# Optimization experiments

Measured on AMD Instinct MI355X. Metric: run time of the kernel, lower is better.

## Reference

```python
import jax, jax.numpy as jnp
import numpy as np

T = 8          # number of adapter tasks
H = 1024       # hidden_size
I = 4096       # intermediate_size (bert dense input)
D = H // 16    # adapter bottleneck (reduction_factor=16)
B, S = 8, 512
EPS = 1e-12    # BERT LayerNorm eps


def _layernorm(x, g, b):
    mu = jnp.mean(x, axis=-1, keepdims=True)
    var = jnp.mean(jnp.square(x - mu), axis=-1, keepdims=True)
    return (x - mu) * jax.lax.rsqrt(var + EPS) * g + b


def setup_inputs() -> dict:
    key = jax.random.key(0)
    ks = jax.random.split(key, 14)
    std = 0.02
    inp = {
        "hidden_states": jax.random.normal(ks[0], (B, S, I), jnp.float32),
        "input_tensor": jax.random.normal(ks[1], (B, S, H), jnp.float32),
        "dense_w": jax.random.normal(ks[2], (H, I), jnp.float32) * std,
        "dense_b": jnp.zeros((H,), jnp.float32),
        "ln_g": jnp.ones((H,), jnp.float32),
        "ln_b": jnp.zeros((H,), jnp.float32),
        "down_w": jax.random.normal(ks[3], (T, D, H), jnp.float32) * std,
        "down_b": jnp.zeros((T, D), jnp.float32),
        "up_w": jax.random.normal(ks[4], (T, H, D), jnp.float32) * std,
        "up_b": jnp.zeros((T, H), jnp.float32),
        "key_w": jax.random.normal(ks[5], (H, H), jnp.float32) * std,
        "key_b": jnp.zeros((H,), jnp.float32),
        "query_w": jax.random.normal(ks[6], (H, H), jnp.float32) * std,
        "query_b": jnp.zeros((H,), jnp.float32),
        # value init: near-zero with identity diagonal
        "value_w": jnp.full((H, H), 1e-6, jnp.float32).at[jnp.arange(H), jnp.arange(H)].set(1.0),
    }
    return inp


def reference(hidden_states, input_tensor, dense_w, dense_b, ln_g, ln_b,
              down_w, down_b, up_w, up_b, key_w, key_b, query_w, query_b, value_w):
    # dense: [B,S,I] @ [H,I]^T -> [B,S,H]   (dropout = identity in eval)
    h = jnp.einsum('bsi,hi->bsh', hidden_states, dense_w) + dense_b
    prenorm = input_tensor + h
    adapter_in = _layernorm(prenorm, ln_g, ln_b)
    # batched per-task adapters: down-project, relu, up-project -> [T,B,S,H]
    down = jax.nn.relu(jnp.einsum('bsh,tdh->tbsd', adapter_in, down_w)
                       + down_b[:, None, None, :])
    adapter_out = jnp.einsum('tbsd,thd->tbsh', down, up_w) + up_b[:, None, None, :]
    # fusion attention over task axis T
    key = jnp.einsum('tbsh,kh->tbsk', adapter_out, key_w) + key_b
    value = jnp.einsum('tbsh,vh->tbsv', adapter_out + h[None], value_w)
    query = jnp.einsum('bsh,qh->bsq', prenorm, query_w) + query_b
    scores = jnp.sum(query[None] * key, axis=-1, keepdims=True)  # [T,B,S,1]
    probs = jax.nn.softmax(scores, axis=0)
    fusion = jnp.sum(probs * value, axis=0)                       # [B,S,H]
    return _layernorm(input_tensor + fusion, ln_g, ln_b)
```

## Files before the change

### kernel.cpp

```cpp
#include <hip/hip_runtime.h>
#include <cstdint>
#include <cstddef>

typedef float   f32x4 __attribute__((ext_vector_type(4)));
typedef _Float16 f16x8 __attribute__((ext_vector_type(8)));
typedef _Float16 f16x4 __attribute__((ext_vector_type(4)));

#define TOK  4096
#define HID  1024
#define IDIM 4096

#define GLDS16(gp, lp) __builtin_amdgcn_global_load_lds(                      \
    (const __attribute__((address_space(1))) void*)(gp),                      \
    (__attribute__((address_space(3))) void*)(lp), 16, 0, 0)


__global__ __launch_bounds__(256, 4) void gemm_dense(
    const _Float16* __restrict__ A, const _Float16* __restrict__ B,
    int K, int Kchunk, float* __restrict__ part)
{
    __shared__ _Float16 lA[4096];
    __shared__ _Float16 lB[4096];
    const int tid  = threadIdx.x;
    const int lane = tid & 63;
    const int wave = tid >> 6;
    const int m0   = blockIdx.x * 128;
    const int n0   = blockIdx.y * 128;
    const int kz0  = blockIdx.z * Kchunk;
    const int wM   = (wave & 1) * 64;
    const int wN   = (wave >> 1) * 64;

    const int srow = lane >> 2;
    const int scol = ((lane & 3) ^ ((lane >> 3) & 3)) * 8;
    const _Float16* gA0 = A + (size_t)(m0 + wave * 32 + srow) * K + kz0 + scol;
    const _Float16* gA1 = gA0 + (size_t)16 * K;
    const _Float16* gB0 = B + (size_t)(n0 + wave * 32 + srow) * K + kz0 + scol;
    const _Float16* gB1 = gB0 + (size_t)16 * K;
    _Float16* sA0 = lA + wave * 1024;
    _Float16* sB0 = lB + wave * 1024;

    f32x4 acc[4][4] = {};
    const int fr  = lane & 15;
    const int khr = lane >> 4;
    const int kxo = (khr ^ ((fr >> 1) & 3)) * 8;

    for (int k = 0; k < Kchunk; k += 32) {
        GLDS16(gA0 + k, sA0);
        GLDS16(gA1 + k, sA0 + 512);
        GLDS16(gB0 + k, sB0);
        GLDS16(gB1 + k, sB0 + 512);
        __syncthreads();
        f16x8 afr[4], bfr[4];
#pragma unroll
        for (int mi = 0; mi < 4; ++mi)
            afr[mi] = *(const f16x8*)(lA + (wM + mi * 16 + fr) * 32 + kxo);
#pragma unroll
        for (int ni = 0; ni < 4; ++ni)
            bfr[ni] = *(const f16x8*)(lB + (wN + ni * 16 + fr) * 32 + kxo);
#pragma unroll
        for (int mi = 0; mi < 4; ++mi)
#pragma unroll
            for (int ni = 0; ni < 4; ++ni)
                acc[mi][ni] = __builtin_amdgcn_mfma_f32_16x16x32_f16(
                    afr[mi], bfr[ni], acc[mi][ni], 0, 0, 0);
        __syncthreads();
    }

    float* dst = part + (size_t)blockIdx.z * TOK * HID;
    const int cn = lane & 15;
    const int rq = (lane >> 4) * 4;
#pragma unroll
    for (int mi = 0; mi < 4; ++mi)
#pragma unroll
        for (int r = 0; r < 4; ++r) {
            const int m = m0 + wM + mi * 16 + rq + r;
#pragma unroll
            for (int ni = 0; ni < 4; ++ni) {
                const int n = n0 + wN + ni * 16 + cn;
                dst[(size_t)m * HID + n] = acc[mi][ni][r];
            }
        }
}

template <int MODE>
__global__ __launch_bounds__(1024, 4) void gemm_w32(
    const _Float16* __restrict__ Ah, const _Float16* __restrict__ B,
    int K, int Ncols,
    float* __restrict__ outF, _Float16* __restrict__ outH,
    const float* __restrict__ bias, const float* __restrict__ addv,
    const float* __restrict__ probs, const float* __restrict__ upb,
    const _Float16* __restrict__ A2, const _Float16* __restrict__ B2,
    _Float16* __restrict__ outH2)
{
    __shared__ _Float16 lA[4096];
    __shared__ _Float16 lB[4096];
    const int tid  = threadIdx.x;
    const int lane = tid & 63;
    const int wave = tid >> 6;
    const int m0   = blockIdx.x * 128;
    int n0, half = 0;
    const _Float16* Ap = Ah;
    const _Float16* Bp = B;
    if constexpr (MODE == 5) {
        half = blockIdx.y >> 2;
        n0 = (blockIdx.y & 3) * 128;
        if (half) { Ap = A2; Bp = B2; }
    } else {
        n0 = blockIdx.y * 128;
    }
    const int wM = (wave & 3) * 32;
    const int wN = (wave >> 2) * 32;

    f32x4 acc[2][2] = {};

    const int i8   = wave & 7;
    const int srow = lane >> 2;
    const int scol = ((lane & 3) ^ ((lane >> 3) & 3)) * 8;
    const _Float16* gsrc = ((wave < 8)
        ? Ap + (size_t)(m0 + i8 * 16 + srow) * K
        : Bp + (size_t)(n0 + i8 * 16 + srow) * K) + scol;
    _Float16* ldst = ((wave < 8) ? lA : lB) + i8 * 512;

    const int fr  = lane & 15;
    const int khr = lane >> 4;
    const int kxo = (khr ^ ((fr >> 1) & 3)) * 8;

    for (int k0 = 0; k0 < K; k0 += 32) {
        GLDS16(gsrc + k0, ldst);
        __syncthreads();
        f16x8 afr[2], bfr[2];
#pragma unroll
        for (int mi = 0; mi < 2; ++mi)
            afr[mi] = *(const f16x8*)(lA + (wM + mi * 16 + fr) * 32 + kxo);
#pragma unroll
        for (int ni = 0; ni < 2; ++ni)
            bfr[ni] = *(const f16x8*)(lB + (wN + ni * 16 + fr) * 32 + kxo);
#pragma unroll
        for (int mi = 0; mi < 2; ++mi)
#pragma unroll
            for (int ni = 0; ni < 2; ++ni)
                acc[mi][ni] = __builtin_amdgcn_mfma_f32_16x16x32_f16(
                    afr[mi], bfr[ni], acc[mi][ni], 0, 0, 0);
        __syncthreads();
    }

    const int cn = lane & 15;
    const int rq = (lane >> 4) * 4;
#pragma unroll
    for (int mi = 0; mi < 2; ++mi)
#pragma unroll
        for (int r = 0; r < 4; ++r) {
            const int m = m0 + wM + mi * 16 + rq + r;
#pragma unroll
            for (int ni = 0; ni < 2; ++ni) {
                const int n = n0 + wN + ni * 16 + cn;
                const float v = acc[mi][ni][r];
                if constexpr (MODE == 1) {
                    const float bb = bias ? bias[n] : 0.f;
                    outH[(size_t)m * Ncols + n] = (_Float16)(v + bb);
                } else if constexpr (MODE == 3) {
                    const size_t idx = (size_t)m * Ncols + n;
                    float s = v + addv[idx];
#pragma unroll
                    for (int t = 0; t < 8; ++t)
                        s += probs[(size_t)m * 8 + t] * upb[t * 1024 + n];
                    outH[idx] = (_Float16)s;
                } else if constexpr (MODE == 4) {
                    const size_t idx = (size_t)m * Ncols + n;
                    outF[idx] = v + addv[idx];
                } else {
                    const size_t idx = (size_t)m * 512 + n;
                    if (half == 0) {
                        const float y = v + bias[n];
                        outH[idx] = (_Float16)(y > 0.f ? y : 0.f);
                    } else {
                        outH2[idx] = (_Float16)v;
                    }
                }
            }
        }
}

__global__ __launch_bounds__(256) void ln_fused(
    const float* __restrict__ part, int sk,
    const float* __restrict__ dbias, const float* __restrict__ it,
    const float* __restrict__ gam, const float* __restrict__ bet,
    float* __restrict__ h_f32, _Float16* __restrict__ ai, _Float16* __restrict__ pn)
{
    const int n = blockIdx.x, tid = threadIdx.x;
    const int lane = tid & 63, wave = tid >> 6;
    const size_t base = (size_t)n * 1024 + tid * 4;
    f32x4 h = *(const f32x4*)(dbias + tid * 4);
    for (int z = 0; z < sk; ++z)
        h += *(const f32x4*)(part + (size_t)z * TOK * HID + base);
    *(f32x4*)(h_f32 + base) = h;
    f32x4 x = h + *(const f32x4*)(it + base);
    float s = x[0] + x[1] + x[2] + x[3];
    float q = x[0] * x[0] + x[1] * x[1] + x[2] * x[2] + x[3] * x[3];
#pragma unroll
    for (int off = 1; off < 64; off <<= 1) {
        s += __shfl_xor(s, off);
        q += __shfl_xor(q, off);
    }
    __shared__ float rs[4], rq[4];
    if (lane == 0) { rs[wave] = s; rq[wave] = q; }
    __syncthreads();
    s = rs[0] + rs[1] + rs[2] + rs[3];
    q = rq[0] + rq[1] + rq[2] + rq[3];
    const float mu = s * (1.f / 1024.f);
    const float var = q * (1.f / 1024.f) - mu * mu;
    const float rstd = rsqrtf(var + 1e-12f);
    f32x4 gv = *(const f32x4*)(gam + tid * 4);
    f32x4 bv = *(const f32x4*)(bet + tid * 4);
    f16x4 av, pv;
#pragma unroll
    for (int j = 0; j < 4; ++j) {
        const float y = (x[j] - mu) * rstd * gv[j] + bv[j];
        av[j] = (_Float16)y;
        pv[j] = (_Float16)x[j];
    }
    *(f16x4*)(ai + base) = av;
    *(f16x4*)(pn + base) = pv;
}

__global__ __launch_bounds__(256) void ln_out(
    const float* __restrict__ fuse, const float* __restrict__ gam,
    const float* __restrict__ bet, float* __restrict__ outp)
{
    const int n = blockIdx.x, tid = threadIdx.x;
    const int lane = tid & 63, wave = tid >> 6;
    const size_t base = (size_t)n * 1024 + tid * 4;
    f32x4 x = *(const f32x4*)(fuse + base);
    float s = x[0] + x[1] + x[2] + x[3];
    float q = x[0] * x[0] + x[1] * x[1] + x[2] * x[2] + x[3] * x[3];
#pragma unroll
    for (int off = 1; off < 64; off <<= 1) {
        s += __shfl_xor(s, off);
        q += __shfl_xor(q, off);
    }
    __shared__ float rs[4], rq[4];
    if (lane == 0) { rs[wave] = s; rq[wave] = q; }
    __syncthreads();
    s = rs[0] + rs[1] + rs[2] + rs[3];
    q = rq[0] + rq[1] + rq[2] + rq[3];
    const float mu = s * (1.f / 1024.f);
    const float var = q * (1.f / 1024.f) - mu * mu;
    const float rstd = rsqrtf(var + 1e-12f);
    f32x4 gv = *(const f32x4*)(gam + tid * 4);
    f32x4 bv = *(const f32x4*)(bet + tid * 4);
    f32x4 y;
#pragma unroll
    for (int j = 0; j < 4; ++j) y[j] = (x[j] - mu) * rstd * gv[j] + bv[j];
    *(f32x4*)(outp + base) = y;
}

__global__ __launch_bounds__(256) void scores_softmax(
    const _Float16* __restrict__ qk, const float* __restrict__ up_b,
    const _Float16* __restrict__ down, const _Float16* __restrict__ g,
    float* __restrict__ probs_out, _Float16* __restrict__ wdown)
{
    const int n = blockIdx.x, tid = threadIdx.x;
    const int lane = tid & 63, wave = tid >> 6;
    const _Float16* qkrow = qk + (size_t)n * 1024;
    float ub[8] = {};
#pragma unroll
    for (int j = 0; j < 4; ++j) {
        const int h = tid + j * 256;
        const float qkv = (float)qkrow[h];
#pragma unroll
        for (int t = 0; t < 8; ++t) ub[t] += qkv * up_b[t * 1024 + h];
    }
#pragma unroll
    for (int off = 1; off < 64; off <<= 1) {
#pragma unroll
        for (int t = 0; t < 8; ++t) ub[t] += __shfl_xor(ub[t], off);
    }
    __shared__ float red[4][9];
    __shared__ float sd[8];
    __shared__ float pl[8];
    if (lane == 0) {
#pragma unroll
        for (int t = 0; t < 8; ++t) red[wave][t] = ub[t];
    }
    const int c0 = tid * 2;
    const size_t dbase = (size_t)n * 512;
    const float d0 = (float)down[dbase + c0];
    const float d1 = (float)down[dbase + c0 + 1];
    float pz = d0 * (float)g[dbase + c0] + d1 * (float)g[dbase + c0 + 1];
#pragma unroll
    for (int off = 1; off < 32; off <<= 1) pz += __shfl_xor(pz, off);
    if ((lane & 31) == 0) sd[wave * 2 + (lane >> 5)] = pz;
    __syncthreads();
    if (tid == 0) {
        float sc[8];
        float mx = -1e30f;
#pragma unroll
        for (int t = 0; t < 8; ++t) {
            sc[t] = sd[t] + red[0][t] + red[1][t] + red[2][t] + red[3][t];
            mx = fmaxf(mx, sc[t]);
        }
        float sum = 0.f;
#pragma unroll
        for (int t = 0; t < 8; ++t) { sc[t] = expf(sc[t] - mx); sum += sc[t]; }
        const float inv = 1.f / sum;
#pragma unroll
        for (int t = 0; t < 8; ++t) pl[t] = sc[t] * inv;
    }
    __syncthreads();
    const float pr = pl[c0 >> 6];
    wdown[dbase + c0]     = (_Float16)(pr * d0);
    wdown[dbase + c0 + 1] = (_Float16)(pr * d1);
    if (tid < 8) probs_out[(size_t)n * 8 + tid] = pl[tid];
}

__device__ inline void cvt_seg(const float* __restrict__ s, _Float16* __restrict__ d,
                               int n4, int gid, int gsz)
{
    for (int i = gid; i < n4; i += gsz) {
        f32x4 v = ((const f32x4*)s)[i];
        f16x4 o;
        o[0] = (_Float16)v[0]; o[1] = (_Float16)v[1];
        o[2] = (_Float16)v[2]; o[3] = (_Float16)v[3];
        ((f16x4*)d)[i] = o;
    }
}

__global__ __launch_bounds__(256) void convert4(
    const float* s0, _Float16* d0, int n0,
    const float* s1, _Float16* d1, int n1,
    const float* s2, _Float16* d2, int n2,
    const float* s3, _Float16* d3, int n3,
    float* bz)
{
    if (blockIdx.x == 0) {
        f32x4 z = {0.f, 0.f, 0.f, 0.f};
        *(f32x4*)(bz + threadIdx.x * 4) = z;
    }
    const int gid = blockIdx.x * 256 + threadIdx.x;
    const int gsz = gridDim.x * 256;
    cvt_seg(s0, d0, n0, gid, gsz);
    cvt_seg(s1, d1, n1, gid, gsz);
    cvt_seg(s2, d2, n2, gid, gsz);
    cvt_seg(s3, d3, n3, gid, gsz);
}

__global__ __launch_bounds__(256) void transpose_kw(
    const float* __restrict__ in, _Float16* __restrict__ outp,
    const float* __restrict__ rvec, float* __restrict__ rout)
{
    __shared__ float t[32][33];
    __shared__ float rpart[8][33];
    const int bx = blockIdx.x * 32;
    const int by = blockIdx.y * 32;
    const int tx = threadIdx.x & 31, ty = threadIdx.x >> 5;
#pragma unroll
    for (int j = 0; j < 32; j += 8)
        t[ty + j][tx] = in[(size_t)(by + ty + j) * 1024 + bx + tx];
    __syncthreads();
#pragma unroll
    for (int j = 0; j < 32; j += 8)
        outp[(size_t)(bx + ty + j) * 1024 + by + tx] = (_Float16)t[tx][ty + j];
    if (rvec) {
        float s = 0.f;
#pragma unroll
        for (int j = 0; j < 4; ++j) {
            const int k = ty * 4 + j;
            s += rvec[by + k] * t[k][tx];
        }
        rpart[ty][tx] = s;
        __syncthreads();
        if (ty == 0) {
            float v = rpart[0][tx];
#pragma unroll
            for (int r = 1; r < 8; ++r) v += rpart[r][tx];
            atomicAdd(rout + bx + tx, v);
        }
    }
}

__global__ __launch_bounds__(256) void reshape_up(
    const float* __restrict__ up_w, _Float16* __restrict__ upg,
    _Float16* __restrict__ upmix)
{
    const int i = blockIdx.x * 256 + threadIdx.x;
    const int d = i & 63;
    const int h = (i >> 6) & 1023;
    const int t = i >> 16;
    const float v = up_w[i];
    upg[(size_t)(t * 64 + d) * 1024 + h] = (_Float16)v;
    upmix[(size_t)h * 512 + t * 64 + d]  = (_Float16)v;
}

extern "C" void kernel_launch(void* const* d_in, const int* in_sizes, int n_in,
                              void* d_out, int out_size, void* d_ws, size_t ws_size,
                              hipStream_t stream)
{
    const float* hs      = (const float*)d_in[0];
    const float* it      = (const float*)d_in[1];
    const float* dense_w = (const float*)d_in[2];
    const float* dense_b = (const float*)d_in[3];
    const float* ln_g    = (const float*)d_in[4];
    const float* ln_b    = (const float*)d_in[5];
    const float* down_w  = (const float*)d_in[6];
    const float* down_b  = (const float*)d_in[7];
    const float* up_w    = (const float*)d_in[8];
    const float* up_b    = (const float*)d_in[9];
    const float* key_w   = (const float*)d_in[10];
    const float* key_b   = (const float*)d_in[11];
    const float* query_w = (const float*)d_in[12];
    const float* query_b = (const float*)d_in[13];
    const float* value_w = (const float*)d_in[14];
    float* outp = (float*)d_out;
    (void)in_sizes; (void)n_in; (void)out_size; (void)key_b;

    const size_t MiB = 1ull << 20;
    char* p = (char*)d_ws;
    _Float16* w_dense  = (_Float16*)p; p += 8 * MiB;
    _Float16* w_queryT = (_Float16*)p; p += 2 * MiB;
    _Float16* w_keyT   = (_Float16*)p; p += 2 * MiB;
    _Float16* w_value  = (_Float16*)p; p += 2 * MiB;
    _Float16* w_fuseT  = (_Float16*)p; p += 2 * MiB;
    _Float16* w_down   = (_Float16*)p; p += 1 * MiB;
    _Float16* w_upg    = (_Float16*)p; p += 1 * MiB;
    _Float16* w_upmix  = (_Float16*)p; p += 1 * MiB;
    float*    bfuse    = (float*)p;    p += 1 * MiB;
    float*    h_f32    = (float*)p;    p += 16 * MiB;
    _Float16* ai       = (_Float16*)p; p += 8 * MiB;
    _Float16* pn       = (_Float16*)p; p += 8 * MiB;
    _Float16* hs_h = (_Float16*)h_f32;
    char* rb = p;
    const int sk = (ws_size >= (size_t)(52 + 64) * MiB) ? 4 : 2;
    float*    part  = (float*)rb;
    _Float16* qk    = (_Float16*)(rb +  8 * MiB);
    _Float16* down  = (_Float16*)(rb + 16 * MiB);
    _Float16* g     = (_Float16*)(rb + 20 * MiB);
    _Float16* wdown = (_Float16*)(rb + 24 * MiB);
    float*    probs = (float*)(rb + 28 * MiB);
    float*    fuse  = (float*)rb;
    _Float16* mixed = ai;

    convert4<<<2048, 256, 0, stream>>>(hs, hs_h, TOK * IDIM / 4,
                                       dense_w, w_dense, HID * IDIM / 4,
                                       value_w, w_value, HID * HID / 4,
                                       down_w,  w_down,  512 * HID / 4,
                                       bfuse);
    transpose_kw<<<dim3(32, 32), 256, 0, stream>>>(key_w, w_keyT, query_b, bfuse);
    transpose_kw<<<dim3(32, 32), 256, 0, stream>>>(query_w, w_queryT, nullptr, nullptr);
    reshape_up<<<2048, 256, 0, stream>>>(up_w, w_upg, w_upmix);
    gemm_w32<1><<<dim3(8, 8), 1024, 0, stream>>>(
        w_keyT, w_queryT, HID, HID, nullptr, w_fuseT, nullptr, nullptr, nullptr,
        nullptr, nullptr, nullptr, nullptr);

    gemm_dense<<<dim3(32, 8, sk), 256, 0, stream>>>(hs_h, w_dense, IDIM, IDIM / sk, part);
    ln_fused<<<TOK, 256, 0, stream>>>(part, sk, dense_b, it, ln_g, ln_b, h_f32, ai, pn);
    gemm_w32<1><<<dim3(32, 8), 1024, 0, stream>>>(
        pn, w_fuseT, HID, HID, nullptr, qk, bfuse, nullptr, nullptr, nullptr,
        nullptr, nullptr, nullptr);
    gemm_w32<5><<<dim3(32, 8), 1024, 0, stream>>>(
        ai, w_down, HID, 512, nullptr, down, down_b, nullptr, nullptr, nullptr,
        qk, w_upg, g);
    scores_softmax<<<TOK, 256, 0, stream>>>(qk, up_b, down, g, probs, wdown);
    gemm_w32<3><<<dim3(32, 8), 1024, 0, stream>>>(
        wdown, w_upmix, 512, HID, nullptr, mixed, nullptr, h_f32, probs, up_b,
        nullptr, nullptr, nullptr);
    gemm_w32<4><<<dim3(32, 8), 1024, 0, stream>>>(
        mixed, w_value, HID, HID, fuse, nullptr, nullptr, it, nullptr, nullptr,
        nullptr, nullptr, nullptr);
    ln_out<<<TOK, 256, 0, stream>>>(fuse, ln_g, ln_b, outp);
}
```

Baseline: 362.7 us.

## Double-buffer LDS tiles in dense and w32 GEMM kernels

Both GEMM kernels now keep two LDS buffers and issue the global-to-LDS loads for the next K step before computing on the current one, dropping one barrier per iteration. The aim is to overlap global memory latency with MFMA work. The cost is twice the shared memory per block, which can lower occupancy under the launch bounds. Correctness depends on the direct-to-LDS loads having completed when the single remaining barrier is reached, since no explicit wait on the load counter is added.

Result: faster. 345.2 us (-4.8%).

```diff
diff --git a/kernel.cpp b/kernel.cpp
--- a/kernel.cpp
+++ b/kernel.cpp
@@ -19,8 +19,8 @@
     const _Float16* __restrict__ A, const _Float16* __restrict__ B,
     int K, int Kchunk, float* __restrict__ part)
 {
-    __shared__ _Float16 lA[4096];
-    __shared__ _Float16 lB[4096];
+    __shared__ _Float16 lA[2][4096];
+    __shared__ _Float16 lB[2][4096];
     const int tid  = threadIdx.x;
     const int lane = tid & 63;
     const int wave = tid >> 6;
@@ -36,27 +36,35 @@
     const _Float16* gA1 = gA0 + (size_t)16 * K;
     const _Float16* gB0 = B + (size_t)(n0 + wave * 32 + srow) * K + kz0 + scol;
     const _Float16* gB1 = gB0 + (size_t)16 * K;
-    _Float16* sA0 = lA + wave * 1024;
-    _Float16* sB0 = lB + wave * 1024;
+    const int soff = wave * 1024;
 
     f32x4 acc[4][4] = {};
     const int fr  = lane & 15;
     const int khr = lane >> 4;
     const int kxo = (khr ^ ((fr >> 1) & 3)) * 8;
 
+    GLDS16(gA0, &lA[0][soff]);
+    GLDS16(gA1, &lA[0][soff + 512]);
+    GLDS16(gB0, &lB[0][soff]);
+    GLDS16(gB1, &lB[0][soff + 512]);
+    __syncthreads();
+
+    int cur = 0;
     for (int k = 0; k < Kchunk; k += 32) {
-        GLDS16(gA0 + k, sA0);
-        GLDS16(gA1 + k, sA0 + 512);
-        GLDS16(gB0 + k, sB0);
-        GLDS16(gB1 + k, sB0 + 512);
-        __syncthreads();
+        if (k + 32 < Kchunk) {
+            const int nb = cur ^ 1;
+            GLDS16(gA0 + k + 32, &lA[nb][soff]);
+            GLDS16(gA1 + k + 32, &lA[nb][soff + 512]);
+            GLDS16(gB0 + k + 32, &lB[nb][soff]);
+            GLDS16(gB1 + k + 32, &lB[nb][soff + 512]);
+        }
         f16x8 afr[4], bfr[4];
 #pragma unroll
         for (int mi = 0; mi < 4; ++mi)
-            afr[mi] = *(const f16x8*)(lA + (wM + mi * 16 + fr) * 32 + kxo);
+            afr[mi] = *(const f16x8*)(&lA[cur][(wM + mi * 16 + fr) * 32 + kxo]);
 #pragma unroll
         for (int ni = 0; ni < 4; ++ni)
-            bfr[ni] = *(const f16x8*)(lB + (wN + ni * 16 + fr) * 32 + kxo);
+            bfr[ni] = *(const f16x8*)(&lB[cur][(wN + ni * 16 + fr) * 32 + kxo]);
 #pragma unroll
         for (int mi = 0; mi < 4; ++mi)
 #pragma unroll
@@ -64,6 +72,7 @@
                 acc[mi][ni] = __builtin_amdgcn_mfma_f32_16x16x32_f16(
                     afr[mi], bfr[ni], acc[mi][ni], 0, 0, 0);
         __syncthreads();
+        cur ^= 1;
     }
 
     float* dst = part + (size_t)blockIdx.z * TOK * HID;
@@ -92,8 +101,8 @@
     const _Float16* __restrict__ A2, const _Float16* __restrict__ B2,
     _Float16* __restrict__ outH2)
 {
-    __shared__ _Float16 lA[4096];
-    __shared__ _Float16 lB[4096];
+    __shared__ _Float16 lA[2][4096];
+    __shared__ _Float16 lB[2][4096];
     const int tid  = threadIdx.x;
     const int lane = tid & 63;
     const int wave = tid >> 6;
@@ -119,22 +128,26 @@
     const _Float16* gsrc = ((wave < 8)
         ? Ap + (size_t)(m0 + i8 * 16 + srow) * K
         : Bp + (size_t)(n0 + i8 * 16 + srow) * K) + scol;
-    _Float16* ldst = ((wave < 8) ? lA : lB) + i8 * 512;
+    _Float16* ldst = ((wave < 8) ? &lA[0][0] : &lB[0][0]) + i8 * 512;
 
     const int fr  = lane & 15;
     const int khr = lane >> 4;
     const int kxo = (khr ^ ((fr >> 1) & 3)) * 8;
 
+    GLDS16(gsrc, ldst);
+    __syncthreads();
+
+    int cur = 0;
     for (int k0 = 0; k0 < K; k0 += 32) {
-        GLDS16(gsrc + k0, ldst);
-        __syncthreads();
+        if (k0 + 32 < K)
+            GLDS16(gsrc + k0 + 32, ldst + (cur ^ 1) * 4096);
         f16x8 afr[2], bfr[2];
 #pragma unroll
         for (int mi = 0; mi < 2; ++mi)
-            afr[mi] = *(const f16x8*)(lA + (wM + mi * 16 + fr) * 32 + kxo);
+            afr[mi] = *(const f16x8*)(&lA[cur][(wM + mi * 16 + fr) * 32 + kxo]);
 #pragma unroll
         for (int ni = 0; ni < 2; ++ni)
-            bfr[ni] = *(const f16x8*)(lB + (wN + ni * 16 + fr) * 32 + kxo);
+            bfr[ni] = *(const f16x8*)(&lB[cur][(wN + ni * 16 + fr) * 32 + kxo]);
 #pragma unroll
         for (int mi = 0; mi < 2; ++mi)
 #pragma unroll
@@ -142,6 +155,7 @@
                 acc[mi][ni] = __builtin_amdgcn_mfma_f32_16x16x32_f16(
                     afr[mi], bfr[ni], acc[mi][ni], 0, 0, 0);
         __syncthreads();
+        cur ^= 1;
     }
 
     const int cn = lane & 15;
```
